# Performance work log

Hardware: AMD Instinct MI355X
Metric: run time of the kernel (lower is better)

Reference implementation:

```python
import jax, jax.numpy as jnp
import numpy as np

EPS = 1e-12  # torch F.normalize default eps


def _l2norm(t, axis=-1):
    n = jnp.sqrt(jnp.sum(t * t, axis=axis, keepdims=True))
    return t / jnp.maximum(n, EPS)


def setup_inputs() -> dict:
    key = jax.random.key(0)
    ks = jax.random.split(key, 5)
    B, N, C, H = 8, 4096, 1024, 16
    x = jax.random.normal(ks[0], (B, N, C), dtype=jnp.float32)
    # nn.Linear(dim, 3*dim, bias=False): weight [3C, C]; we store transposed [C, 3C]
    w_qkv = jax.random.normal(ks[1], (C, 3 * C), dtype=jnp.float32) * (1.0 / np.sqrt(C))
    temperature = jnp.ones((H, 1, 1), dtype=jnp.float32)
    w_proj = jax.random.normal(ks[2], (C, C), dtype=jnp.float32) * (1.0 / np.sqrt(C))
    b_proj = jax.random.normal(ks[3], (C,), dtype=jnp.float32) * 0.01
    return {"x": x, "w_qkv": w_qkv, "temperature": temperature,
            "w_proj": w_proj, "b_proj": b_proj}


def reference(x, w_qkv, temperature, w_proj, b_proj):
    B, N, C = x.shape
    H = temperature.shape[0]
    dh = C // H
    # qkv: [B, N, 3C] -> [B, N, 3, H, dh] -> q/k/v each [B, H, dh, N]
    qkv = (x @ w_qkv).reshape(B, N, 3, H, dh).transpose(2, 0, 3, 4, 1)
    q, k, v = qkv[0], qkv[1], qkv[2]
    # L2-normalize over token axis (last dim)
    q = _l2norm(q)
    k = _l2norm(k)
    # channel-channel attention: [B, H, dh, dh]
    attn = jnp.einsum("bhdn,bhen->bhde", q, k) * temperature  # temp broadcasts [H,1,1]
    attn = jax.nn.softmax(attn, axis=-1)
    # weighted sum over channels: [B, H, dh, N] -> [B, N, C]
    out = jnp.einsum("bhde,bhen->bhdn", attn, v).transpose(0, 3, 1, 2).reshape(B, N, C)
    return out @ w_proj + b_proj
```

## Files before the change

### kernel.cpp

```cpp
#include <hip/hip_runtime.h>
#include <cstdint>

typedef unsigned short u16;
typedef unsigned int u32;
typedef __attribute__((ext_vector_type(8))) short bf16x8;
typedef __attribute__((ext_vector_type(4))) float f32x4;

typedef const u32 __attribute__((address_space(1)))* gp_t;
typedef u32 __attribute__((address_space(3)))* lp_t;

__device__ __forceinline__ u16 f2bf(float f) {
    union { float f; u32 u; } v; v.f = f;
    u32 r = v.u + 0x7FFFu + ((v.u >> 16) & 1u);
    return (u16)(r >> 16);
}
__device__ __forceinline__ float bf2f(u16 h) {
    union { u32 u; float f; } v; v.u = ((u32)h) << 16;
    return v.f;
}

__global__ void k_pack_x(const float* __restrict__ x, u16* __restrict__ xb, int n4) {
    int stride = gridDim.x * blockDim.x;
    for (int i = blockIdx.x * blockDim.x + threadIdx.x; i < n4; i += stride) {
        float4 v = ((const float4*)x)[i];
        ushort4 o;
        o.x = f2bf(v.x); o.y = f2bf(v.y); o.z = f2bf(v.z); o.w = f2bf(v.w);
        ((ushort4*)xb)[i] = o;
    }
}

__global__ void k_transpose_w(const float* __restrict__ src, u16* __restrict__ dst, int ncols) {
    __shared__ float t[64][65];
    int ntn = ncols >> 6;
    int kb = (blockIdx.x / ntn) * 64;
    int nb = (blockIdx.x % ntn) * 64;
    for (int i = threadIdx.x; i < 4096; i += 256) {
        int r = i >> 6, c = i & 63;
        t[r][c] = src[(long)(kb + r) * ncols + nb + c];
    }
    __syncthreads();
    for (int i = threadIdx.x; i < 4096; i += 256) {
        int r = i >> 6, c = i & 63;
        dst[(long)(nb + r) * 1024 + kb + c] = f2bf(t[c][r]);
    }
}

__global__ __launch_bounds__(256) void k_pack_wv(const float* __restrict__ wqkv, u16* __restrict__ wvb) {
    const int idx = blockIdx.x * 256 + threadIdx.x;
    const int cin = idx >> 7, e0 = (idx & 127) * 8;
    const float4 v1 = *(const float4*)(wqkv + (long)cin * 3072 + 2048 + e0);
    const float4 v2 = *(const float4*)(wqkv + (long)cin * 3072 + 2048 + e0 + 4);
    u16 u[8];
    u[0] = f2bf(v1.x); u[1] = f2bf(v1.y); u[2] = f2bf(v1.z); u[3] = f2bf(v1.w);
    u[4] = f2bf(v2.x); u[5] = f2bf(v2.y); u[6] = f2bf(v2.z); u[7] = f2bf(v2.w);
    *(uint4*)(wvb + (long)cin * 1024 + e0) = *(const uint4*)u;
}

template<int EPI>
__global__ __launch_bounds__(512, 2) void k_gemm(
    const u16* __restrict__ A, const u16* __restrict__ Bt,
    int nTilesN,
    u16* __restrict__ qkT, u16* __restrict__ v_tm,
    float* __restrict__ outp, const float* __restrict__ bias)
{
    __shared__ uint4 smem4[8704];
    u16* sm = (u16*)smem4;

    const int tid = threadIdx.x;
    const int wid = tid >> 6, lane = tid & 63;
    const int wr = wid >> 2, wc = wid & 3;
    const int fr = lane & 15, sl = lane >> 4;

    const int nwg = gridDim.x;
    const int cpx = nwg >> 3;
    const int logical = (blockIdx.x & 7) * cpx + (blockIdx.x >> 3);

    const int bn = logical % nTilesN;
    const long m0 = (long)(logical / nTilesN) * 256;
    const int n0 = bn * 256;

    const int srow = wid * 32 + (lane >> 2);
    const int kswz = (((lane & 3) ^ ((srow >> 1) & 3)) << 3);
    const u16* gA = A + (m0 + srow) * 1024L + kswz;
    const u16* gB = Bt + ((long)n0 + srow) * 1024L + kswz;
    const int ldst = wid * 1024;

    const int fxor = ((sl ^ ((fr >> 1) & 3)) << 3);
    const int aBase = (wr * 128 + fr) * 32 + fxor;
    const int bBase = 32768 + (wc * 64 + fr) * 32 + fxor;

    f32x4 acc[8][4];
#pragma unroll
    for (int i = 0; i < 8; ++i)
#pragma unroll
        for (int j = 0; j < 4; ++j) acc[i][j] = (f32x4){0.f, 0.f, 0.f, 0.f};

#define STAGE_A(d, kh, ts) do { \
    const u16* g_ = gA + (ts) * 64 + (kh) * 32; \
    u16* l_ = sm + (d) * 16384 + (kh) * 8192 + ldst; \
    __builtin_amdgcn_global_load_lds((gp_t)g_, (lp_t)l_, 16, 0, 0); \
    __builtin_amdgcn_global_load_lds((gp_t)(g_ + 16 * 1024), (lp_t)(l_ + 512), 16, 0, 0); \
} while (0)
#define STAGE_B(d, kh, ts) do { \
    const u16* g_ = gB + (ts) * 64 + (kh) * 32; \
    u16* l_ = sm + 32768 + (d) * 16384 + (kh) * 8192 + ldst; \
    __builtin_amdgcn_global_load_lds((gp_t)g_, (lp_t)l_, 16, 0, 0); \
    __builtin_amdgcn_global_load_lds((gp_t)(g_ + 16 * 1024), (lp_t)(l_ + 512), 16, 0, 0); \
} while (0)

    STAGE_A(0, 0, 0); STAGE_B(0, 0, 0);
    STAGE_A(0, 1, 0); STAGE_B(0, 1, 0);
    STAGE_A(1, 0, 1); STAGE_B(1, 0, 1);
    asm volatile("s_waitcnt vmcnt(8)" ::: "memory");
    __builtin_amdgcn_s_barrier();

    bf16x8 afX[4], afY[4], bfX[4], bfY[4];
#pragma unroll
    for (int ni = 0; ni < 4; ++ni) bfX[ni] = *(const bf16x8*)(sm + bBase + ni * 512);
#pragma unroll
    for (int mi = 0; mi < 4; ++mi) afX[mi] = *(const bf16x8*)(sm + aBase + mi * 512);

#pragma unroll 2
    for (int T = 0; T < 16; ++T) {
        const int d = T & 1;
        const int t1 = (T + 1 < 16) ? T + 1 : 15;
        const int t2 = (T + 2 < 16) ? T + 2 : 15;
        const int base = d * 16384;
        const int nbase = (d ^ 1) * 16384;

#pragma unroll
        for (int mi = 0; mi < 4; ++mi)
            afY[mi] = *(const bf16x8*)(sm + aBase + (4 + mi) * 512 + base);
        STAGE_A(d ^ 1, 1, t1);
        asm volatile("s_waitcnt vmcnt(6)" ::: "memory");
        __builtin_amdgcn_s_barrier();
        __builtin_amdgcn_s_setprio(1);
#pragma unroll
// ... 9 lines not shown
            bfY[ni] = *(const bf16x8*)(sm + bBase + ni * 512 + base + 8192);
#pragma unroll
        for (int mi = 0; mi < 4; ++mi)
            afX[mi] = *(const bf16x8*)(sm + aBase + mi * 512 + base + 8192);
        STAGE_B(d ^ 1, 1, t1);
        __builtin_amdgcn_s_barrier();
        __builtin_amdgcn_s_setprio(1);
#pragma unroll
        for (int mi = 0; mi < 4; ++mi)
#pragma unroll
            for (int ni = 0; ni < 4; ++ni)
                acc[mi + 4][ni] = __builtin_amdgcn_mfma_f32_16x16x32_bf16(afY[mi], bfX[ni], acc[mi + 4][ni], 0, 0, 0);
        __builtin_amdgcn_s_setprio(0);
        __builtin_amdgcn_s_barrier();

#pragma unroll
        for (int mi = 0; mi < 4; ++mi)
            afY[mi] = *(const bf16x8*)(sm + aBase + (4 + mi) * 512 + base + 8192);
        STAGE_A(d, 0, t2);
        asm volatile("s_waitcnt vmcnt(6)" ::: "memory");
        __builtin_amdgcn_s_barrier();
        __builtin_amdgcn_s_setprio(1);
#pragma unroll
        for (int mi = 0; mi < 4; ++mi)
#pragma unroll
            for (int ni = 0; ni < 4; ++ni)
                acc[mi][ni] = __builtin_amdgcn_mfma_f32_16x16x32_bf16(afX[mi], bfY[ni], acc[mi][ni], 0, 0, 0);
        __builtin_amdgcn_s_setprio(0);
        __builtin_amdgcn_s_barrier();

#pragma unroll
        for (int ni = 0; ni < 4; ++ni)
            bfX[ni] = *(const bf16x8*)(sm + bBase + ni * 512 + nbase);
#pragma unroll
        for (int mi = 0; mi < 4; ++mi)
            afX[mi] = *(const bf16x8*)(sm + aBase + mi * 512 + nbase);
        STAGE_B(d, 0, t2);
        __builtin_amdgcn_s_barrier();
        __builtin_amdgcn_s_setprio(1);
#pragma unroll
        for (int mi = 0; mi < 4; ++mi)
#pragma unroll
            for (int ni = 0; ni < 4; ++ni)
                acc[mi + 4][ni] = __builtin_amdgcn_mfma_f32_16x16x32_bf16(afY[mi], bfY[ni], acc[mi + 4][ni], 0, 0, 0);
        __builtin_amdgcn_s_setprio(0);
        __builtin_amdgcn_s_barrier();
    }
#undef STAGE_A
#undef STAGE_B
    asm volatile("s_waitcnt vmcnt(0)" ::: "memory");
    __syncthreads();

    if (EPI == 0) {
        const long b = m0 >> 12;
        const int tok0 = (int)(m0 & 4095);
        u16* piece = sm + wid * 8704;
#pragma unroll
        for (int mi = 0; mi < 8; ++mi)
#pragma unroll
            for (int ni = 0; ni < 4; ++ni) {
                const int ch = ni * 16 + fr;
                const int tk = mi * 16 + sl * 4;
                ushort4 w;
                w.x = f2bf(acc[mi][ni][0]); w.y = f2bf(acc[mi][ni][1]);
                w.z = f2bf(acc[mi][ni][2]); w.w = f2bf(acc[mi][ni][3]);
                *(ushort4*)(piece + ch * 136 + tk) = w;
            }
        __syncthreads();
#pragma unroll
        for (int i = 0; i < 16; ++i) {
            const int chunk = i * 512 + tid;
            const int row = chunk >> 4, c16 = chunk & 15;
            const int p = row >> 6, chl = row & 63;
            const int wrp = p >> 2, wcp = p & 3;
            const uint4 v = *(const uint4*)(sm + p * 8704 + chl * 136 + c16 * 8);
            *(uint4*)(qkT + ((b * 2048 + n0 + wcp * 64 + chl) * 4096L + tok0 + wrp * 128 + c16 * 8)) = v;
        }
    }
}

__global__ __launch_bounds__(512, 2) void k_gram(
    const u16* __restrict__ qkT, float* __restrict__ gram_part, float* __restrict__ sq_part)
{
    __shared__ u16 lQ[64 * 256];
    __shared__ u16 lK[64 * 256];

    const int blk = blockIdx.x;
    const int seg = blk & 15;
    const int bh = blk >> 4;
    const int b = bh >> 4, h = bh & 15;
    const int tid = threadIdx.x;
    const int wid = tid >> 6, lane = tid & 63;

    {
        const int r2 = lane >> 5;
        const int slot = lane & 31;
        const int rbase = wid * 8;
#pragma unroll
        for (int i = 0; i < 4; ++i) {
            const int r = rbase + i * 2 + r2;
            const int col = seg * 256 + ((slot ^ (r & 7)) << 3);
            const u16* gq = qkT + ((long)(b * 2048 + h * 64 + r)) * 4096 + col;
            const u16* gk = qkT + ((long)(b * 2048 + 1024 + h * 64 + r)) * 4096 + col;
            __builtin_amdgcn_global_load_lds((gp_t)gq, (lp_t)(lQ + (rbase + i * 2) * 256), 16, 0, 0);
            __builtin_amdgcn_global_load_lds((gp_t)gk, (lp_t)(lK + (rbase + i * 2) * 256), 16, 0, 0);
        }
    }
    __syncthreads();

    {
        const int row = tid >> 2, q4 = tid & 3;
        const u16* src = (row < 64 ? lQ + row * 256 : lK + (row - 64) * 256) + q4 * 64;
        float s = 0.f;
#pragma unroll
        for (int i = 0; i < 8; ++i) {
            uint4 v = *(const uint4*)(src + i * 8);
            float a0, a1;
            a0 = bf2f((u16)(v.x & 0xFFFF)); a1 = bf2f((u16)(v.x >> 16)); s += a0 * a0 + a1 * a1;
            a0 = bf2f((u16)(v.y & 0xFFFF)); a1 = bf2f((u16)(v.y >> 16)); s += a0 * a0 + a1 * a1;
            a0 = bf2f((u16)(v.z & 0xFFFF)); a1 = bf2f((u16)(v.z >> 16)); s += a0 * a0 + a1 * a1;
            a0 = bf2f((u16)(v.w & 0xFFFF)); a1 = bf2f((u16)(v.w >> 16)); s += a0 * a0 + a1 * a1;
        }
        s += __shfl_xor(s, 1);
        s += __shfl_xor(s, 2);
        if (q4 == 0) sq_part[(long)blk * 128 + row] = s;
    }

    const int mrow = wid >> 1, npair = wid & 1;
    const int fr = lane & 15, sl = lane >> 4;
    f32x4 acc[2];
    acc[0] = (f32x4){0.f, 0.f, 0.f, 0.f};
    acc[1] = (f32x4){0.f, 0.f, 0.f, 0.f};
#pragma unroll
    for (int ks = 0; ks < 8; ++ks) {
        const int ra = mrow * 16 + fr;
        const bf16x8 a = *(const bf16x8*)(lQ + ra * 256 + (((ks * 4 + sl) ^ (ra & 7)) << 3));
#pragma unroll
        for (int ni = 0; ni < 2; ++ni) {
            const int rb = npair * 32 + ni * 16 + fr;
            const bf16x8 bb = *(const bf16x8*)(lK + rb * 256 + (((ks * 4 + sl) ^ (rb & 7)) << 3));
            acc[ni] = __builtin_amdgcn_mfma_f32_16x16x32_bf16(a, bb, acc[ni], 0, 0, 0);
        }
    }
    float* gp = gram_part + (long)blk * 4096;
#pragma unroll
    for (int ni = 0; ni < 2; ++ni)
#pragma unroll
        for (int r = 0; r < 4; ++r)
            gp[(mrow * 16 + sl * 4 + r) * 64 + npair * 32 + ni * 16 + fr] = acc[ni][r];
}

__global__ __launch_bounds__(256) void k_smax(
    const float* __restrict__ gram_part, const float* __restrict__ sq_part,
    const float* __restrict__ temperature, u16* __restrict__ attn_g)
{
    const int row = blockIdx.x * 4 + (threadIdx.x >> 6);
    const int e = threadIdx.x & 63;
    const int bh = row >> 6, d = row & 63;
    const int h = bh & 15;
    float raw = 0.f, sqq = 0.f, sqk = 0.f;
    const float* gp = gram_part + (long)bh * 16 * 4096 + d * 64 + e;
    const float* sp = sq_part + (long)bh * 16 * 128;
#pragma unroll
    for (int s = 0; s < 16; ++s) {
        raw += gp[s * 4096];
        sqq += sp[s * 128 + d];
        sqk += sp[s * 128 + 64 + e];
    }
    const float rq = 1.f / fmaxf(sqrtf(sqq), 1e-12f);
    const float rk = 1.f / fmaxf(sqrtf(sqk), 1e-12f);
    const float v = raw * rq * rk * temperature[h];
    float mx = v;
#pragma unroll
    for (int o = 32; o; o >>= 1) mx = fmaxf(mx, __shfl_xor(mx, o));
    const float p = __expf(v - mx);
    float sum = p;
#pragma unroll
    for (int o = 32; o; o >>= 1) sum += __shfl_xor(sum, o);
    attn_g[(long)row * 64 + e] = f2bf(p / sum);
}

__global__ __launch_bounds__(256) void k_wmix(
    const u16* __restrict__ attn_g, const u16* __restrict__ wpT, u16* __restrict__ wmix)
{
    __shared__ u16 lA[64 * 72];
    __shared__ u16 lB[256 * 64];

    const int blk = blockIdx.x;
    const int nseg = blk & 3, bh = blk >> 2;
    const int b = bh >> 4, h = bh & 15;
    const int tid = threadIdx.x;
    const int wid = tid >> 6, lane = tid & 63;
    const int fr = lane & 15, sl = lane >> 4;

#pragma unroll
    for (int i = 0; i < 8; ++i) {
        const int cc = wid * 8 + i;
        const int row = cc * 8 + (lane >> 3);
        const int slot = lane & 7;
        const u16* g = wpT + (long)(nseg * 256 + row) * 1024 + h * 64 + ((slot ^ (row & 7)) << 3);
        __builtin_amdgcn_global_load_lds((gp_t)g, (lp_t)(lB + cc * 512), 16, 0, 0);
    }
    {
        const u16* src = attn_g + (long)bh * 4096;
        for (int i = tid; i < 4096; i += 256) {
            const int d = i >> 6, e = i & 63;
            lA[e * 72 + d] = src[i];
        }
    }
    __syncthreads();

    f32x4 acc[4][4];
#pragma unroll
    for (int i = 0; i < 4; ++i)
#pragma unroll
        for (int j = 0; j < 4; ++j) acc[i][j] = (f32x4){0.f, 0.f, 0.f, 0.f};

#pragma unroll
    for (int ks = 0; ks < 2; ++ks) {
        bf16x8 a[4], bb[4];
#pragma unroll
        for (int mi = 0; mi < 4; ++mi)
            a[mi] = *(const bf16x8*)(lA + (mi * 16 + fr) * 72 + ks * 32 + sl * 8);
#pragma unroll
        for (int ni = 0; ni < 4; ++ni) {
            const int rb = wid * 64 + ni * 16 + fr;
            bb[ni] = *(const bf16x8*)(lB + rb * 64 + (((ks * 4 + sl) ^ (rb & 7)) << 3));
        }
#pragma unroll
        for (int mi = 0; mi < 4; ++mi)
#pragma unroll
            for (int ni = 0; ni < 4; ++ni)
                acc[mi][ni] = __builtin_amdgcn_mfma_f32_16x16x32_bf16(a[mi], bb[ni], acc[mi][ni], 0, 0, 0);
    }

    u16* dst = wmix + ((long)b << 20);
#pragma unroll
    for (int mi = 0; mi < 4; ++mi)
#pragma unroll
        for (int ni = 0; ni < 4; ++ni) {
            const int cout = nseg * 256 + wid * 64 + ni * 16 + fr;
            const int e0 = mi * 16 + sl * 4;
            ushort4 w;
            w.x = f2bf(acc[mi][ni][0]); w.y = f2bf(acc[mi][ni][1]);
            w.z = f2bf(acc[mi][ni][2]); w.w = f2bf(acc[mi][ni][3]);
            *(ushort4*)(dst + (long)cout * 1024 + h * 64 + e0) = w;
        }
}

__global__ __launch_bounds__(256) void k_g128(
    const u16* __restrict__ A, long Ab, const u16* __restrict__ Bt, long Bs,
    u16* __restrict__ C, long Cb, int K, int MT, int NT)
{
    __shared__ u16 sm[8192];
    __shared__ u16 lC[128 * 136];

    const int tid = threadIdx.x;
    const int wid = tid >> 6, lane = tid & 63;
    const int wr = wid >> 1, wc = wid & 1;
    const int fr = lane & 15, sl = lane >> 4;

    const int nwg = gridDim.x;
    const int logical = (blockIdx.x & 7) * (nwg >> 3) + (blockIdx.x >> 3);

    const int b = logical / (MT * NT);
    const int r = logical % (MT * NT);
    const int i0 = r / NT, j0 = r % NT;
    const int m0 = i0 * 128, n0 = j0 * 128;
    const u16* Abp = A + (long)b * Ab;
    const u16* Bbp = Bt + (long)b * Bs;
    u16* Cbp = C + (long)b * Cb;

    const int srow = lane >> 2;
    const int sslot = lane & 3;

    f32x4 acc[4][4];
#pragma unroll
    for (int i = 0; i < 4; ++i)
#pragma unroll
        for (int j = 0; j < 4; ++j) acc[i][j] = (f32x4){0.f, 0.f, 0.f, 0.f};

    for (int kt = 0; kt < K; kt += 32) {
        __syncthreads();
#pragma unroll
        for (int i = 0; i < 2; ++i) {
            const int row = wid * 32 + i * 16 + srow;
            const int swz = (sslot ^ ((row >> 1) & 3)) << 3;
            const u16* ga = Abp + (long)(m0 + row) * K + kt + swz;
            const u16* gb = Bbp + (long)(n0 + row) * K + kt + swz;
            __builtin_amdgcn_global_load_lds((gp_t)ga, (lp_t)(sm + (wid * 2 + i) * 512), 16, 0, 0);
            __builtin_amdgcn_global_load_lds((gp_t)gb, (lp_t)(sm + 4096 + (wid * 2 + i) * 512), 16, 0, 0);
        }
        __syncthreads();
        bf16x8 af[4], bfr[4];
#pragma unroll
        for (int mi = 0; mi < 4; ++mi) {
            const int row = wr * 64 + mi * 16 + fr;
            af[mi] = *(const bf16x8*)(sm + row * 32 + ((sl ^ ((row >> 1) & 3)) << 3));
        }
#pragma unroll
        for (int ni = 0; ni < 4; ++ni) {
            const int row = wc * 64 + ni * 16 + fr;
            bfr[ni] = *(const bf16x8*)(sm + 4096 + row * 32 + ((sl ^ ((row >> 1) & 3)) << 3));
        }
#pragma unroll
        for (int mi = 0; mi < 4; ++mi)
#pragma unroll
            for (int ni = 0; ni < 4; ++ni)
                acc[mi][ni] = __builtin_amdgcn_mfma_f32_16x16x32_bf16(af[mi], bfr[ni], acc[mi][ni], 0, 0, 0);
    }
    __syncthreads();

#pragma unroll
    for (int mi = 0; mi < 4; ++mi)
#pragma unroll
        for (int ni = 0; ni < 4; ++ni) {
            const int ch = wc * 64 + ni * 16 + fr;
            const int tk = wr * 64 + mi * 16 + sl * 4;
#pragma unroll
            for (int rr = 0; rr < 4; ++rr)
                lC[(tk + rr) * 136 + ch] = f2bf(acc[mi][ni][rr]);
        }
    __syncthreads();
    {
        const int tk = tid >> 1, half = tid & 1;
        const u16* sp = lC + tk * 136 + half * 64;
        u16* dp = Cbp + (long)(m0 + tk) * 1024 + n0 + half * 64;
#pragma unroll
        for (int i = 0; i < 8; ++i) ((uint4*)dp)[i] = ((const uint4*)sp)[i];
    }
}

__global__ __launch_bounds__(512, 2) void k_gemm256f(
    const u16* __restrict__ A, long Ab, const u16* __restrict__ Bt, long Bs,
    int MT, int NT, float* __restrict__ cF, long Cb, const float* __restrict__ bias)
{
    __shared__ uint4 smem4[8704];
    u16* sm = (u16*)smem4;

    const int tid = threadIdx.x;
    const int wid = tid >> 6, lane = tid & 63;
    const int wr = wid >> 2, wc = wid & 3;
    const int fr = lane & 15, sl = lane >> 4;

    const int nwg = gridDim.x;
    const int logical = (blockIdx.x & 7) * (nwg >> 3) + (blockIdx.x >> 3);
    const int b = logical / (MT * NT);
    const int rem = logical % (MT * NT);
    const int mt = rem / NT, nt = rem % NT;
    const long m0 = (long)mt * 256;
    const int n0 = nt * 256;

    const int srow = wid * 32 + (lane >> 2);
    const int kswz = (((lane & 3) ^ ((srow >> 1) & 3)) << 3);
    const u16* gA = A + (long)b * Ab + (m0 + srow) * 1024L + kswz;
    const u16* gB = Bt + (long)b * Bs + ((long)n0 + srow) * 1024L + kswz;
    const int ldst = wid * 1024;

    const int fxor = ((sl ^ ((fr >> 1) & 3)) << 3);
    const int aBase = (wr * 128 + fr) * 32 + fxor;
    const int bBase = 32768 + (wc * 64 + fr) * 32 + fxor;

    f32x4 acc[8][4];
#pragma unroll
    for (int i = 0; i < 8; ++i)
#pragma unroll
        for (int j = 0; j < 4; ++j) acc[i][j] = (f32x4){0.f, 0.f, 0.f, 0.f};

#define STAGE_A(d, kh, ts) do { \
    const u16* g_ = gA + (ts) * 64 + (kh) * 32; \
    u16* l_ = sm + (d) * 16384 + (kh) * 8192 + ldst; \
    __builtin_amdgcn_global_load_lds((gp_t)g_, (lp_t)l_, 16, 0, 0); \
    __builtin_amdgcn_global_load_lds((gp_t)(g_ + 16 * 1024), (lp_t)(l_ + 512), 16, 0, 0); \
} while (0)
#define STAGE_B(d, kh, ts) do { \
    const u16* g_ = gB + (ts) * 64 + (kh) * 32; \
    u16* l_ = sm + 32768 + (d) * 16384 + (kh) * 8192 + ldst; \
    __builtin_amdgcn_global_load_lds((gp_t)g_, (lp_t)l_, 16, 0, 0); \
    __builtin_amdgcn_global_load_lds((gp_t)(g_ + 16 * 1024), (lp_t)(l_ + 512), 16, 0, 0); \
} while (0)

    STAGE_A(0, 0, 0); STAGE_B(0, 0, 0);
    STAGE_A(0, 1, 0); STAGE_B(0, 1, 0);
    STAGE_A(1, 0, 1); STAGE_B(1, 0, 1);
    asm volatile("s_waitcnt vmcnt(8)" ::: "memory");
    __builtin_amdgcn_s_barrier();

    bf16x8 afX[4], afY[4], bfX[4], bfY[4];
#pragma unroll
    for (int ni = 0; ni < 4; ++ni) bfX[ni] = *(const bf16x8*)(sm + bBase + ni * 512);
#pragma unroll
    for (int mi = 0; mi < 4; ++mi) afX[mi] = *(const bf16x8*)(sm + aBase + mi * 512);

#pragma unroll 2
    for (int T = 0; T < 16; ++T) {
        const int d = T & 1;
        const int t1 = (T + 1 < 16) ? T + 1 : 15;
        const int t2 = (T + 2 < 16) ? T + 2 : 15;
        const int base = d * 16384;
        const int nbase = (d ^ 1) * 16384;

#pragma unroll
        for (int mi = 0; mi < 4; ++mi)
            afY[mi] = *(const bf16x8*)(sm + aBase + (4 + mi) * 512 + base);
        STAGE_A(d ^ 1, 1, t1);
        asm volatile("s_waitcnt vmcnt(6)" ::: "memory");
        __builtin_amdgcn_s_barrier();
        __builtin_amdgcn_s_setprio(1);
#pragma unroll
        for (int mi = 0; mi < 4; ++mi)
#pragma unroll
            for (int ni = 0; ni < 4; ++ni)
                acc[mi][ni] = __builtin_amdgcn_mfma_f32_16x16x32_bf16(afX[mi], bfX[ni], acc[mi][ni], 0, 0, 0);
        __builtin_amdgcn_s_setprio(0);
        __builtin_amdgcn_s_barrier();

#pragma unroll
        for (int ni = 0; ni < 4; ++ni)
            bfY[ni] = *(const bf16x8*)(sm + bBase + ni * 512 + base + 8192);
#pragma unroll
        for (int mi = 0; mi < 4; ++mi)
            afX[mi] = *(const bf16x8*)(sm + aBase + mi * 512 + base + 8192);
        STAGE_B(d ^ 1, 1, t1);
        __builtin_amdgcn_s_barrier();
        __builtin_amdgcn_s_setprio(1);
#pragma unroll
        for (int mi = 0; mi < 4; ++mi)
#pragma unroll
            for (int ni = 0; ni < 4; ++ni)
                acc[mi + 4][ni] = __builtin_amdgcn_mfma_f32_16x16x32_bf16(afY[mi], bfX[ni], acc[mi + 4][ni], 0, 0, 0);
        __builtin_amdgcn_s_setprio(0);
        __builtin_amdgcn_s_barrier();

#pragma unroll
        for (int mi = 0; mi < 4; ++mi)
            afY[mi] = *(const bf16x8*)(sm + aBase + (4 + mi) * 512 + base + 8192);
        STAGE_A(d, 0, t2);
        asm volatile("s_waitcnt vmcnt(6)" ::: "memory");
        __builtin_amdgcn_s_barrier();
        __builtin_amdgcn_s_setprio(1);
#pragma unroll
        for (int mi = 0; mi < 4; ++mi)
#pragma unroll
            for (int ni = 0; ni < 4; ++ni)
                acc[mi][ni] = __builtin_amdgcn_mfma_f32_16x16x32_bf16(afX[mi], bfY[ni], acc[mi][ni], 0, 0, 0);
        __builtin_amdgcn_s_setprio(0);
        __builtin_amdgcn_s_barrier();

#pragma unroll
        for (int ni = 0; ni < 4; ++ni)
            bfX[ni] = *(const bf16x8*)(sm + bBase + ni * 512 + nbase);
#pragma unroll
        for (int mi = 0; mi < 4; ++mi)
            afX[mi] = *(const bf16x8*)(sm + aBase + mi * 512 + nbase);
        STAGE_B(d, 0, t2);
        __builtin_amdgcn_s_barrier();
        __builtin_amdgcn_s_setprio(1);
#pragma unroll
        for (int mi = 0; mi < 4; ++mi)
#pragma unroll
            for (int ni = 0; ni < 4; ++ni)
                acc[mi + 4][ni] = __builtin_amdgcn_mfma_f32_16x16x32_bf16(afY[mi], bfY[ni], acc[mi + 4][ni], 0, 0, 0);
        __builtin_amdgcn_s_setprio(0);
        __builtin_amdgcn_s_barrier();
    }
#undef STAGE_A
#undef STAGE_B
    asm volatile("s_waitcnt vmcnt(0)" ::: "memory");
    __syncthreads();

    float* cbase = cF + (long)b * Cb;
    float bi[4];
#pragma unroll
    for (int ni = 0; ni < 4; ++ni) bi[ni] = bias[n0 + wc * 64 + ni * 16 + fr];
#pragma unroll
    for (int pass = 0; pass < 2; ++pass) {
        float* pieceF = (float*)smem4 + wid * 4352;
        if (pass) __syncthreads();
#pragma unroll
        for (int mi2 = 0; mi2 < 4; ++mi2) {
            const int mi = pass * 4 + mi2;
#pragma unroll
            for (int ni = 0; ni < 4; ++ni) {
                const int ch = ni * 16 + fr;
                const int tk = mi2 * 16 + sl * 4;
#pragma unroll
                for (int rr = 0; rr < 4; ++rr)
                    pieceF[(tk + rr) * 68 + ch] = acc[mi][ni][rr] + bi[ni];
            }
        }
        __syncthreads();
#pragma unroll
        for (int i = 0; i < 16; ++i) {
            const int chunk = i * 512 + tid;
            const int row = chunk >> 4, c4 = chunk & 15;
            const int p = row >> 6, tk = row & 63;
            const int wrp = p >> 2, wcp = p & 3;
            const float4 v = *(const float4*)((float*)smem4 + p * 4352 + tk * 68 + c4 * 4);
            *(float4*)(cbase + (m0 + wrp * 128 + pass * 64 + tk) * 1024L + n0 + wcp * 64 + c4 * 4) = v;
        }
    }
}

extern "C" void kernel_launch(void* const* d_in, const int* in_sizes, int n_in,
                              void* d_out, int out_size, void* d_ws, size_t ws_size,
                              hipStream_t stream) {
    const float* x = (const float*)d_in[0];
    const float* w_qkv = (const float*)d_in[1];
    const float* temperature = (const float*)d_in[2];
    const float* w_proj = (const float*)d_in[3];
    const float* b_proj = (const float*)d_in[4];
    float* out = (float*)d_out;
    char* ws = (char*)d_ws;

    u16* wqT    = (u16*)(ws);
    u16* wpT    = (u16*)(ws + 6291456);
    u16* wvb    = (u16*)(ws + 8388608);
    u16* xt     = (u16*)(ws + 10485760);
    u16* qkT    = (u16*)(ws + 77594624);
    float* gram_part = (float*)(ws + 211812352);
    float* sq_part   = (float*)(ws + 245366784);
    u16* attn_g = (u16*)(ws + 246415360);
    u16* wmix   = (u16*)(ws + 247463936);
    u16* wfinT  = (u16*)(ws + 211812352);

    k_pack_x<<<2048, 256, 0, stream>>>(x, xt, 8388608);
    k_transpose_w<<<768, 256, 0, stream>>>(w_qkv, wqT, 3072);
    k_transpose_w<<<256, 256, 0, stream>>>(w_proj, wpT, 1024);
    k_pack_wv<<<512, 256, 0, stream>>>(w_qkv, wvb);
    k_gemm<0><<<1024, 512, 0, stream>>>(xt, wqT, 8, qkT, nullptr, nullptr, nullptr);
    k_gram<<<2048, 512, 0, stream>>>(qkT, gram_part, sq_part);
    k_smax<<<2048, 256, 0, stream>>>(gram_part, sq_part, temperature, attn_g);
    k_wmix<<<512, 256, 0, stream>>>(attn_g, wpT, wmix);
    k_g128<<<512, 256, 0, stream>>>(wmix, 1048576L, wvb, 0L, wfinT, 1048576L, 1024, 8, 8);
    k_gemm256f<<<512, 512, 0, stream>>>(xt, 4194304L, wfinT, 1048576L, 16, 4, out, 4194304L, b_proj);
}
```

Baseline: 358.6 us.

## Compute gram via input covariance X^T X instead of materializing Q/K projections

Replaces the large QK projection GEMM over all tokens with a symmetric per-batch covariance S = X^T X (1024x1024), then forms U = S·Wqk and gets the Q·K gram and the row norms as Wq^T·U contractions. A new pack kernel writes x in both token-major and channel-major bf16 layouts so the symmetric GEMM can read it. The goal is to drop the B·N×2C projection, its writeback and the partial-gram reductions. In exchange it adds a transpose pass over x and an extra intermediate, and accumulating S and U in bf16 may change numerical accuracy.

```diff
diff --git a/kernel.cpp b/kernel.cpp
--- a/kernel.cpp
+++ b/kernel.cpp
@@ -19,13 +19,40 @@
     return v.f;
 }
 
-__global__ void k_pack_x(const float* __restrict__ x, u16* __restrict__ xb, int n4) {
-    int stride = gridDim.x * blockDim.x;
-    for (int i = blockIdx.x * blockDim.x + threadIdx.x; i < n4; i += stride) {
-        float4 v = ((const float4*)x)[i];
-        ushort4 o;
-        o.x = f2bf(v.x); o.y = f2bf(v.y); o.z = f2bf(v.z); o.w = f2bf(v.w);
-        ((ushort4*)xb)[i] = o;
+__global__ __launch_bounds__(256) void k_pack2(const float* __restrict__ x,
+                                               u16* __restrict__ xt, u16* __restrict__ xc) {
+    __shared__ u16 tb[64][72];
+    const int blk = blockIdx.x;
+    const int tt = blk >> 4, ct = blk & 15;
+    const long tok0 = (long)tt * 64;
+    const int ch0 = ct * 64;
+    const int tid = threadIdx.x;
+    const int row = tid >> 2, cq = tid & 3;
+#pragma unroll
+    for (int jj = 0; jj < 4; ++jj) {
+        const float4 v = *(const float4*)(x + (tok0 + row) * 1024 + ch0 + cq * 16 + jj * 4);
+        tb[row][cq * 16 + jj * 4 + 0] = f2bf(v.x);
+        tb[row][cq * 16 + jj * 4 + 1] = f2bf(v.y);
+        tb[row][cq * 16 + jj * 4 + 2] = f2bf(v.z);
+        tb[row][cq * 16 + jj * 4 + 3] = f2bf(v.w);
+    }
+    __syncthreads();
+#pragma unroll
+    for (int s = 0; s < 2; ++s) {
+        const int c = s * 256 + tid;
+        const int r2 = c >> 3, col8 = c & 7;
+        *(uint4*)(xt + (tok0 + r2) * 1024 + ch0 + col8 * 8) = *(const uint4*)(&tb[r2][col8 * 8]);
+    }
+    const int b = (int)(tok0 >> 12);
+    const int nin = (int)(tok0 & 4095);
+#pragma unroll
+    for (int s = 0; s < 2; ++s) {
+        const int c = s * 256 + tid;
+        const int crow = c >> 3, t8 = c & 7;
+        u16 u[8];
+#pragma unroll
+        for (int k = 0; k < 8; ++k) u[k] = tb[t8 * 8 + k][crow];
+        *(uint4*)(xc + ((long)b * 1024 + ch0 + crow) * 4096 + nin + t8 * 8) = *(const uint4*)u;
     }
 }
 
@@ -56,12 +83,125 @@
     *(uint4*)(wvb + (long)cin * 1024 + e0) = *(const uint4*)u;
 }
 
+template<int SYM>
+__global__ __launch_bounds__(256) void k_g128(
+    const u16* __restrict__ A, long Ab, const u16* __restrict__ Bt, long Bs,
+    u16* __restrict__ C, long Cb, int K, int MT, int NT)
+{
+    __shared__ u16 sm[8192];
+    __shared__ u16 lC[128 * 136];
+
+    const int tid = threadIdx.x;
+    const int wid = tid >> 6, lane = tid & 63;
+    const int wr = wid >> 1, wc = wid & 1;
+    const int fr = lane & 15, sl = lane >> 4;
+
+    const int nwg = gridDim.x;
+    const int logical = (blockIdx.x & 7) * (nwg >> 3) + (blockIdx.x >> 3);
+
+    int b, i0, j0;
+    if (SYM) {
+        const int per = MT * (MT + 1) / 2;
+        b = logical / per;
+        int t = logical % per;
+        int i = 0;
+        while (t >= MT - i) { t -= MT - i; ++i; }
+        i0 = i; j0 = i + t;
+    } else {
+        b = logical / (MT * NT);
+        const int r = logical % (MT * NT);
+        i0 = r / NT; j0 = r % NT;
+    }
+    const int m0 = i0 * 128, n0 = j0 * 128;
+    const u16* Abp = A + (long)b * Ab;
+    const u16* Bbp = Bt + (long)b * Bs;
+    u16* Cbp = C + (long)b * Cb;
+
+    const int srow = lane >> 2;
+    const int sslot = lane & 3;
+
+    f32x4 acc[4][4];
+#pragma unroll
+    for (int i = 0; i < 4; ++i)
+#pragma unroll
+        for (int j = 0; j < 4; ++j) acc[i][j] = (f32x4){0.f, 0.f, 0.f, 0.f};
+
+    for (int kt = 0; kt < K; kt += 32) {
+        __syncthreads();
+#pragma unroll
+        for (int i = 0; i < 2; ++i) {
+            const int row = wid * 32 + i * 16 + srow;
+            const int swz = (sslot ^ ((row >> 1) & 3)) << 3;
+            const u16* ga = Abp + (long)(m0 + row) * K + kt + swz;
+            const u16* gb = Bbp + (long)(n0 + row) * K + kt + swz;
+            __builtin_amdgcn_global_load_lds((gp_t)ga, (lp_t)(sm + (wid * 2 + i) * 512), 16, 0, 0);
+            __builtin_amdgcn_global_load_lds((gp_t)gb, (lp_t)(sm + 4096 + (wid * 2 + i) * 512), 16, 0, 0);
+        }
+        __syncthreads();
+        bf16x8 af[4], bfr[4];
+#pragma unroll
+        for (int mi = 0; mi < 4; ++mi) {
+            const int row = wr * 64 + mi * 16 + fr;
+            af[mi] = *(const bf16x8*)(sm + row * 32 + ((sl ^ ((row >> 1) & 3)) << 3));
+        }
+#pragma unroll
+        for (int ni = 0; ni < 4; ++ni) {
+            const int row = wc * 64 + ni * 16 + fr;
+            bfr[ni] = *(const bf16x8*)(sm + 4096 + row * 32 + ((sl ^ ((row >> 1) & 3)) << 3));
+        }
+#pragma unroll
+        for (int mi = 0; mi < 4; ++mi)
+#pragma unroll
+            for (int ni = 0; ni < 4; ++ni)
+                acc[mi][ni] = __builtin_amdgcn_mfma_f32_16x16x32_bf16(af[mi], bfr[ni], acc[mi][ni], 0, 0, 0);
+    }
+    __syncthreads();
+
+#pragma unroll
+    for (int mi = 0; mi < 4; ++mi)
+#pragma unroll
+        for (int ni = 0; ni < 4; ++ni) {
+            const int ch = wc * 64 + ni * 16 + fr;
+            const int tk = wr * 64 + mi * 16 + sl * 4;
+#pragma unroll
+            for (int rr = 0; rr < 4; ++rr)
+                lC[(tk + rr) * 136 + ch] = f2bf(acc[mi][ni][rr]);
+        }
+    __syncthreads();
+    {
+        const int tk = tid >> 1, half = tid & 1;
+        const u16* sp = lC + tk * 136 + half * 64;
+        u16* dp = Cbp + (long)(m0 + tk) * 1024 + n0 + half * 64;
+#pragma unroll
+        for (int i = 0; i < 8; ++i) ((uint4*)dp)[i] = ((const uint4*)sp)[i];
+    }
+    if (SYM && i0 != j0) {
+        __syncthreads();
+#pragma unroll
+        for (int mi = 0; mi < 4; ++mi)
+#pragma unroll
+            for (int ni = 0; ni < 4; ++ni) {
+                const int ch = wc * 64 + ni * 16 + fr;
+                const int tk = wr * 64 + mi * 16 + sl * 4;
+                ushort4 w;
+                w.x = f2bf(acc[mi][ni][0]); w.y = f2bf(acc[mi][ni][1]);
+                w.z = f2bf(acc[mi][ni][2]); w.w = f2bf(acc[mi][ni][3]);
+                *(ushort4*)(lC + ch * 136 + tk) = w;
+            }
+        __syncthreads();
+        const int rw = tid >> 1, half = tid & 1;
+        const u16* sp = lC + rw * 136 + half * 64;
+        u16* dp = Cbp + (long)(n0 + rw) * 1024 + m0 + half * 64;
+#pragma unroll
+        for (int i = 0; i < 8; ++i) ((uint4*)dp)[i] = ((const uint4*)sp)[i];
+    }
+}
+
 template<int EPI>
-__global__ __launch_bounds__(512, 2) void k_gemm(
-    const u16* __restrict__ A, const u16* __restrict__ Bt,
-    int nTilesN,
-    u16* __restrict__ qkT, u16* __restrict__ v_tm,
-    float* __restrict__ outp, const float* __restrict__ bias)
+__global__ __launch_bounds__(512, 2) void k_gemm256(
+    const u16* __restrict__ A, long Ab, const u16* __restrict__ Bt, long Bs,
+    int MT, int NT,
+    u16* __restrict__ cB, float* __restrict__ cF, long Cb, const float* __restrict__ bias)
 {
     __shared__ uint4 smem4[8704];
     u16* sm = (u16*)smem4;
@@ -72,17 +212,17 @@
     const int fr = lane & 15, sl = lane >> 4;
 
     const int nwg = gridDim.x;
-    const int cpx = nwg >> 3;
-    const int logical = (blockIdx.x & 7) * cpx + (blockIdx.x >> 3);
-
-    const int bn = logical % nTilesN;
-    const long m0 = (long)(logical / nTilesN) * 256;
-    const int n0 = bn * 256;
+    const int logical = (blockIdx.x & 7) * (nwg >> 3) + (blockIdx.x >> 3);
+    const int b = logical / (MT * NT);
+    const int rem = logical % (MT * NT);
+    const int mt = rem / NT, nt = rem % NT;
+    const long m0 = (long)mt * 256;
+    const int n0 = nt * 256;
 
     const int srow = wid * 32 + (lane >> 2);
     const int kswz = (((lane & 3) ^ ((srow >> 1) & 3)) << 3);
-    const u16* gA = A + (m0 + srow) * 1024L + kswz;
-    const u16* gB = Bt + ((long)n0 + srow) * 1024L + kswz;
+    const u16* gA = A + (long)b * Ab + (m0 + srow) * 1024L + kswz;
+    const u16* gB = Bt + (long)b * Bs + ((long)n0 + srow) * 1024L + kswz;
     const int ldst = wid * 1024;
 
     const int fxor = ((sl ^ ((fr >> 1) & 3)) << 3);
@@ -198,8 +338,7 @@
     __syncthreads();
 
     if (EPI == 0) {
-        const long b = m0 >> 12;
-        const int tok0 = (int)(m0 & 4095);
+        u16* cbase = cB + (long)b * Cb;
         u16* piece = sm + wid * 8704;
 #pragma unroll
         for (int mi = 0; mi < 8; ++mi)
@@ -207,123 +346,130 @@
             for (int ni = 0; ni < 4; ++ni) {
                 const int ch = ni * 16 + fr;
                 const int tk = mi * 16 + sl * 4;
-                ushort4 w;
-                w.x = f2bf(acc[mi][ni][0]); w.y = f2bf(acc[mi][ni][1]);
-                w.z = f2bf(acc[mi][ni][2]); w.w = f2bf(acc[mi][ni][3]);
-                *(ushort4*)(piece + ch * 136 + tk) = w;
+#pragma unroll
+                for (int rr = 0; rr < 4; ++rr)
+                    piece[(tk + rr) * 68 + ch] = f2bf(acc[mi][ni][rr]);
             }
         __syncthreads();
 #pragma unroll
-        for (int i = 0; i < 16; ++i) {
+        for (int i = 0; i < 32; ++i) {
             const int chunk = i * 512 + tid;
-            const int row = chunk >> 4, c16 = chunk & 15;
-            const int p = row >> 6, chl = row & 63;
+            const int row = chunk >> 4, c8 = chunk & 15;
+            const int p = row >> 7, tk = row & 127;
             const int wrp = p >> 2, wcp = p & 3;
-            const uint4 v = *(const uint4*)(sm + p * 8704 + chl * 136 + c16 * 8);
-            *(uint4*)(qkT + ((b * 2048 + n0 + wcp * 64 + chl) * 4096L + tok0 + wrp * 128 + c16 * 8)) = v;
-        }
-    }
-}
-
-__global__ __launch_bounds__(512, 2) void k_gram(
-    const u16* __restrict__ qkT, float* __restrict__ gram_part, float* __restrict__ sq_part)
+            const uint2 v = *(const uint2*)(sm + p * 8704 + tk * 68 + c8 * 4);
+            *(uint2*)(cbase + (m0 + wrp * 128 + tk) * 1024L + n0 + wcp * 64 + c8 * 4) = v;
+        }
+    } else {
+        float* cbase = cF + (long)b * Cb;
+        float bi[4];
+#pragma unroll
+        for (int ni = 0; ni < 4; ++ni) bi[ni] = bias[n0 + wc * 64 + ni * 16 + fr];
+#pragma unroll
+        for (int pass = 0; pass < 2; ++pass) {
+            float* pieceF = (float*)smem4 + wid * 4352;
+            if (pass) __syncthreads();
+#pragma unroll
+            for (int mi2 = 0; mi2 < 4; ++mi2) {
+                const int mi = pass * 4 + mi2;
+#pragma unroll
+                for (int ni = 0; ni < 4; ++ni) {
+                    const int ch = ni * 16 + fr;
+                    const int tk = mi2 * 16 + sl * 4;
+#pragma unroll
+                    for (int rr = 0; rr < 4; ++rr)
+                        pieceF[(tk + rr) * 68 + ch] = acc[mi][ni][rr] + bi[ni];
+                }
+            }
+            __syncthreads();
+#pragma unroll
+            for (int i = 0; i < 16; ++i) {
+                const int chunk = i * 512 + tid;
+                const int row = chunk >> 4, c4 = chunk & 15;
+                const int p = row >> 6, tk = row & 63;
+                const int wrp = p >> 2, wcp = p & 3;
+                const float4 v = *(const float4*)((float*)smem4 + p * 4352 + tk * 68 + c4 * 4);
+                *(float4*)(cbase + (m0 + wrp * 128 + pass * 64 + tk) * 1024L + n0 + wcp * 64 + c4 * 4) = v;
+            }
+        }
+    }
+}
+
+__global__ __launch_bounds__(256) void k_gram2(
+    const u16* __restrict__ wqT, const u16* __restrict__ Ut,
+    const float* __restrict__ temperature, u16* __restrict__ attn_g)
 {
-    __shared__ u16 lQ[64 * 256];
-    __shared__ u16 lK[64 * 256];
-
-    const int blk = blockIdx.x;
-    const int seg = blk & 15;
-    const int bh = blk >> 4;
+    __shared__ float lS[64 * 65];
+    __shared__ float lsq[128];
+
+    const int bh = blockIdx.x;
     const int b = bh >> 4, h = bh & 15;
     const int tid = threadIdx.x;
     const int wid = tid >> 6, lane = tid & 63;
+    const int fr = lane & 15, sl = lane >> 4;
 
     {
-        const int r2 = lane >> 5;
-        const int slot = lane & 31;
-        const int rbase = wid * 8;
-#pragma unroll
-        for (int i = 0; i < 4; ++i) {
-            const int r = rbase + i * 2 + r2;
-            const int col = seg * 256 + ((slot ^ (r & 7)) << 3);
-            const u16* gq = qkT + ((long)(b * 2048 + h * 64 + r)) * 4096 + col;
-            const u16* gk = qkT + ((long)(b * 2048 + 1024 + h * 64 + r)) * 4096 + col;
-            __builtin_amdgcn_global_load_lds((gp_t)gq, (lp_t)(lQ + (rbase + i * 2) * 256), 16, 0, 0);
-            __builtin_amdgcn_global_load_lds((gp_t)gk, (lp_t)(lK + (rbase + i * 2) * 256), 16, 0, 0);
-        }
-    }
-    __syncthreads();
-
-    {
-        const int row = tid >> 2, q4 = tid & 3;
-        const u16* src = (row < 64 ? lQ + row * 256 : lK + (row - 64) * 256) + q4 * 64;
+        const int row = tid >> 1, half = tid & 1;
+        const int j = (row < 64) ? (h * 64 + row) : (1024 + h * 64 + (row - 64));
+        const u16* pa = wqT + (long)j * 1024 + half * 512;
+        const u16* pb = Ut + ((long)b * 2048 + j) * 1024 + half * 512;
         float s = 0.f;
-#pragma unroll
-        for (int i = 0; i < 8; ++i) {
-            uint4 v = *(const uint4*)(src + i * 8);
-            float a0, a1;
-            a0 = bf2f((u16)(v.x & 0xFFFF)); a1 = bf2f((u16)(v.x >> 16)); s += a0 * a0 + a1 * a1;
-            a0 = bf2f((u16)(v.y & 0xFFFF)); a1 = bf2f((u16)(v.y >> 16)); s += a0 * a0 + a1 * a1;
-            a0 = bf2f((u16)(v.z & 0xFFFF)); a1 = bf2f((u16)(v.z >> 16)); s += a0 * a0 + a1 * a1;
-            a0 = bf2f((u16)(v.w & 0xFFFF)); a1 = bf2f((u16)(v.w >> 16)); s += a0 * a0 + a1 * a1;
+#pragma unroll 4
+        for (int i = 0; i < 64; ++i) {
+            const uint4 a = *(const uint4*)(pa + i * 8);
+            const uint4 bv = *(const uint4*)(pb + i * 8);
+            s += bf2f((u16)(a.x & 0xFFFF)) * bf2f((u16)(bv.x & 0xFFFF));
+            s += bf2f((u16)(a.x >> 16))    * bf2f((u16)(bv.x >> 16));
+            s += bf2f((u16)(a.y & 0xFFFF)) * bf2f((u16)(bv.y & 0xFFFF));
+            s += bf2f((u16)(a.y >> 16))    * bf2f((u16)(bv.y >> 16));
+            s += bf2f((u16)(a.z & 0xFFFF)) * bf2f((u16)(bv.z & 0xFFFF));
+            s += bf2f((u16)(a.z >> 16))    * bf2f((u16)(bv.z >> 16));
+            s += bf2f((u16)(a.w & 0xFFFF)) * bf2f((u16)(bv.w & 0xFFFF));
+            s += bf2f((u16)(a.w >> 16))    * bf2f((u16)(bv.w >> 16));
         }
         s += __shfl_xor(s, 1);
-        s += __shfl_xor(s, 2);
-        if (q4 == 0) sq_part[(long)blk * 128 + row] = s;
-    }
-
-    const int mrow = wid >> 1, npair = wid & 1;
-    const int fr = lane & 15, sl = lane >> 4;
-    f32x4 acc[2];
-    acc[0] = (f32x4){0.f, 0.f, 0.f, 0.f};
-    acc[1] = (f32x4){0.f, 0.f, 0.f, 0.f};
-#pragma unroll
-    for (int ks = 0; ks < 8; ++ks) {
-        const int ra = mrow * 16 + fr;
-        const bf16x8 a = *(const bf16x8*)(lQ + ra * 256 + (((ks * 4 + sl) ^ (ra & 7)) << 3));
-#pragma unroll
-        for (int ni = 0; ni < 2; ++ni) {
-            const int rb = npair * 32 + ni * 16 + fr;
-            const bf16x8 bb = *(const bf16x8*)(lK + rb * 256 + (((ks * 4 + sl) ^ (rb & 7)) << 3));
+        if (half == 0) lsq[row] = s;
+    }
+
+    const int d0 = wid * 16;
+    f32x4 acc[4];
+#pragma unroll
+    for (int i = 0; i < 4; ++i) acc[i] = (f32x4){0.f, 0.f, 0.f, 0.f};
+
+    const u16* aRow = wqT + (long)(h * 64 + d0 + fr) * 1024 + sl * 8;
+    const u16* bRow = Ut + ((long)b * 2048 + 1024 + h * 64 + fr) * 1024 + sl * 8;
+#pragma unroll 4
+    for (int kb = 0; kb < 32; ++kb) {
+        const bf16x8 a = *(const bf16x8*)(aRow + kb * 32);
+#pragma unroll
+        for (int ni = 0; ni < 4; ++ni) {
+            const bf16x8 bb = *(const bf16x8*)(bRow + (long)ni * 16384 + kb * 32);
             acc[ni] = __builtin_amdgcn_mfma_f32_16x16x32_bf16(a, bb, acc[ni], 0, 0, 0);
         }
     }
-    float* gp = gram_part + (long)blk * 4096;
-#pragma unroll
-    for (int ni = 0; ni < 2; ++ni)
-#pragma unroll
-        for (int r = 0; r < 4; ++r)
-            gp[(mrow * 16 + sl * 4 + r) * 64 + npair * 32 + ni * 16 + fr] = acc[ni][r];
-}
-
-__global__ __launch_bounds__(256) void k_smax(
-    const float* __restrict__ gram_part, const float* __restrict__ sq_part,
-    const float* __restrict__ temperature, u16* __restrict__ attn_g)
-{
-    const int row = blockIdx.x * 4 + (threadIdx.x >> 6);
-    const int e = threadIdx.x & 63;
-    const int bh = row >> 6, d = row & 63;
-    const int h = bh & 15;
-    float raw = 0.f, sqq = 0.f, sqk = 0.f;
-    const float* gp = gram_part + (long)bh * 16 * 4096 + d * 64 + e;
-    const float* sp = sq_part + (long)bh * 16 * 128;
-#pragma unroll
-    for (int s = 0; s < 16; ++s) {
-        raw += gp[s * 4096];
-        sqq += sp[s * 128 + d];
-        sqk += sp[s * 128 + 64 + e];
-    }
-    const float rq = 1.f / fmaxf(sqrtf(sqq), 1e-12f);
-    const float rk = 1.f / fmaxf(sqrtf(sqk), 1e-12f);
-    const float v = raw * rq * rk * temperature[h];
-    float mx = v;
-#pragma unroll
-    for (int o = 32; o; o >>= 1) mx = fmaxf(mx, __shfl_xor(mx, o));
-    const float p = __expf(v - mx);
-    float sum = p;
-#pragma unroll
-    for (int o = 32; o; o >>= 1) sum += __shfl_xor(sum, o);
-    attn_g[(long)row * 64 + e] = f2bf(p / sum);
+#pragma unroll
+    for (int ni = 0; ni < 4; ++ni)
+#pragma unroll
+        for (int rr = 0; rr < 4; ++rr)
+            lS[(d0 + sl * 4 + rr) * 65 + ni * 16 + fr] = acc[ni][rr];
+    __syncthreads();
+
+    const float temp = temperature[h];
+    const float rk = 1.f / fmaxf(sqrtf(lsq[64 + lane]), 1e-12f);
+#pragma unroll 2
+    for (int i = 0; i < 16; ++i) {
+        const int d = wid * 16 + i;
+        const float rq = 1.f / fmaxf(sqrtf(lsq[d]), 1e-12f);
+        const float v = lS[d * 65 + lane] * rq * rk * temp;
+        float mx = v;
+#pragma unroll
+        for (int o = 32; o; o >>= 1) mx = fmaxf(mx, __shfl_xor(mx, o));
+        const float p = __expf(v - mx);
+        float sum = p;
+#pragma unroll
+        for (int o = 32; o; o >>= 1) sum += __shfl_xor(sum, o);
+        attn_g[(long)bh * 4096 + d * 64 + lane] = f2bf(p / sum);
+    }
 }
 
 __global__ __launch_bounds__(256) void k_wmix(
@@ -392,260 +538,6 @@
             w.z = f2bf(acc[mi][ni][2]); w.w = f2bf(acc[mi][ni][3]);
             *(ushort4*)(dst + (long)cout * 1024 + h * 64 + e0) = w;
         }
-}
-
-__global__ __launch_bounds__(256) void k_g128(
-    const u16* __restrict__ A, long Ab, const u16* __restrict__ Bt, long Bs,
-    u16* __restrict__ C, long Cb, int K, int MT, int NT)
-{
-    __shared__ u16 sm[8192];
-    __shared__ u16 lC[128 * 136];
-
-    const int tid = threadIdx.x;
-    const int wid = tid >> 6, lane = tid & 63;
-    const int wr = wid >> 1, wc = wid & 1;
-    const int fr = lane & 15, sl = lane >> 4;
-
-    const int nwg = gridDim.x;
-    const int logical = (blockIdx.x & 7) * (nwg >> 3) + (blockIdx.x >> 3);
-
-    const int b = logical / (MT * NT);
-    const int r = logical % (MT * NT);
-    const int i0 = r / NT, j0 = r % NT;
-    const int m0 = i0 * 128, n0 = j0 * 128;
-    const u16* Abp = A + (long)b * Ab;
-    const u16* Bbp = Bt + (long)b * Bs;
-    u16* Cbp = C + (long)b * Cb;
-
-    const int srow = lane >> 2;
-    const int sslot = lane & 3;
-
-    f32x4 acc[4][4];
-#pragma unroll
-    for (int i = 0; i < 4; ++i)
-#pragma unroll
-        for (int j = 0; j < 4; ++j) acc[i][j] = (f32x4){0.f, 0.f, 0.f, 0.f};
-
-    for (int kt = 0; kt < K; kt += 32) {
-        __syncthreads();
-#pragma unroll
-        for (int i = 0; i < 2; ++i) {
-            const int row = wid * 32 + i * 16 + srow;
-            const int swz = (sslot ^ ((row >> 1) & 3)) << 3;
-            const u16* ga = Abp + (long)(m0 + row) * K + kt + swz;
-            const u16* gb = Bbp + (long)(n0 + row) * K + kt + swz;
-            __builtin_amdgcn_global_load_lds((gp_t)ga, (lp_t)(sm + (wid * 2 + i) * 512), 16, 0, 0);
-            __builtin_amdgcn_global_load_lds((gp_t)gb, (lp_t)(sm + 4096 + (wid * 2 + i) * 512), 16, 0, 0);
-        }
-        __syncthreads();
-        bf16x8 af[4], bfr[4];
-#pragma unroll
-        for (int mi = 0; mi < 4; ++mi) {
-            const int row = wr * 64 + mi * 16 + fr;
-            af[mi] = *(const bf16x8*)(sm + row * 32 + ((sl ^ ((row >> 1) & 3)) << 3));
-        }
-#pragma unroll
-        for (int ni = 0; ni < 4; ++ni) {
-            const int row = wc * 64 + ni * 16 + fr;
-            bfr[ni] = *(const bf16x8*)(sm + 4096 + row * 32 + ((sl ^ ((row >> 1) & 3)) << 3));
-        }
-#pragma unroll
-        for (int mi = 0; mi < 4; ++mi)
-#pragma unroll
-            for (int ni = 0; ni < 4; ++ni)
-                acc[mi][ni] = __builtin_amdgcn_mfma_f32_16x16x32_bf16(af[mi], bfr[ni], acc[mi][ni], 0, 0, 0);
-    }
-    __syncthreads();
-
-#pragma unroll
-    for (int mi = 0; mi < 4; ++mi)
-#pragma unroll
-        for (int ni = 0; ni < 4; ++ni) {
-            const int ch = wc * 64 + ni * 16 + fr;
-            const int tk = wr * 64 + mi * 16 + sl * 4;
-#pragma unroll
-            for (int rr = 0; rr < 4; ++rr)
-                lC[(tk + rr) * 136 + ch] = f2bf(acc[mi][ni][rr]);
-        }
-    __syncthreads();
-    {
-        const int tk = tid >> 1, half = tid & 1;
-        const u16* sp = lC + tk * 136 + half * 64;
-        u16* dp = Cbp + (long)(m0 + tk) * 1024 + n0 + half * 64;
-#pragma unroll
-        for (int i = 0; i < 8; ++i) ((uint4*)dp)[i] = ((const uint4*)sp)[i];
-    }
-}
-
-__global__ __launch_bounds__(512, 2) void k_gemm256f(
-    const u16* __restrict__ A, long Ab, const u16* __restrict__ Bt, long Bs,
-    int MT, int NT, float* __restrict__ cF, long Cb, const float* __restrict__ bias)
-{
-    __shared__ uint4 smem4[8704];
-    u16* sm = (u16*)smem4;
-
-    const int tid = threadIdx.x;
-    const int wid = tid >> 6, lane = tid & 63;
-    const int wr = wid >> 2, wc = wid & 3;
-    const int fr = lane & 15, sl = lane >> 4;
-
-    const int nwg = gridDim.x;
-    const int logical = (blockIdx.x & 7) * (nwg >> 3) + (blockIdx.x >> 3);
-    const int b = logical / (MT * NT);
-    const int rem = logical % (MT * NT);
-    const int mt = rem / NT, nt = rem % NT;
-    const long m0 = (long)mt * 256;
-    const int n0 = nt * 256;
-
-    const int srow = wid * 32 + (lane >> 2);
-    const int kswz = (((lane & 3) ^ ((srow >> 1) & 3)) << 3);
-    const u16* gA = A + (long)b * Ab + (m0 + srow) * 1024L + kswz;
-    const u16* gB = Bt + (long)b * Bs + ((long)n0 + srow) * 1024L + kswz;
-    const int ldst = wid * 1024;
-
-    const int fxor = ((sl ^ ((fr >> 1) & 3)) << 3);
-    const int aBase = (wr * 128 + fr) * 32 + fxor;
-    const int bBase = 32768 + (wc * 64 + fr) * 32 + fxor;
-
-    f32x4 acc[8][4];
-#pragma unroll
-    for (int i = 0; i < 8; ++i)
-#pragma unroll
-        for (int j = 0; j < 4; ++j) acc[i][j] = (f32x4){0.f, 0.f, 0.f, 0.f};
-
-#define STAGE_A(d, kh, ts) do { \
-    const u16* g_ = gA + (ts) * 64 + (kh) * 32; \
-    u16* l_ = sm + (d) * 16384 + (kh) * 8192 + ldst; \
-    __builtin_amdgcn_global_load_lds((gp_t)g_, (lp_t)l_, 16, 0, 0); \
-    __builtin_amdgcn_global_load_lds((gp_t)(g_ + 16 * 1024), (lp_t)(l_ + 512), 16, 0, 0); \
-} while (0)
-#define STAGE_B(d, kh, ts) do { \
-    const u16* g_ = gB + (ts) * 64 + (kh) * 32; \
-    u16* l_ = sm + 32768 + (d) * 16384 + (kh) * 8192 + ldst; \
-    __builtin_amdgcn_global_load_lds((gp_t)g_, (lp_t)l_, 16, 0, 0); \
-    __builtin_amdgcn_global_load_lds((gp_t)(g_ + 16 * 1024), (lp_t)(l_ + 512), 16, 0, 0); \
-} while (0)
-
-    STAGE_A(0, 0, 0); STAGE_B(0, 0, 0);
-    STAGE_A(0, 1, 0); STAGE_B(0, 1, 0);
-    STAGE_A(1, 0, 1); STAGE_B(1, 0, 1);
-    asm volatile("s_waitcnt vmcnt(8)" ::: "memory");
-    __builtin_amdgcn_s_barrier();
-
-    bf16x8 afX[4], afY[4], bfX[4], bfY[4];
-#pragma unroll
-    for (int ni = 0; ni < 4; ++ni) bfX[ni] = *(const bf16x8*)(sm + bBase + ni * 512);
-#pragma unroll
-    for (int mi = 0; mi < 4; ++mi) afX[mi] = *(const bf16x8*)(sm + aBase + mi * 512);
-
-#pragma unroll 2
-    for (int T = 0; T < 16; ++T) {
-        const int d = T & 1;
-        const int t1 = (T + 1 < 16) ? T + 1 : 15;
-        const int t2 = (T + 2 < 16) ? T + 2 : 15;
-        const int base = d * 16384;
-        const int nbase = (d ^ 1) * 16384;
-
-#pragma unroll
-        for (int mi = 0; mi < 4; ++mi)
-            afY[mi] = *(const bf16x8*)(sm + aBase + (4 + mi) * 512 + base);
-        STAGE_A(d ^ 1, 1, t1);
-        asm volatile("s_waitcnt vmcnt(6)" ::: "memory");
-        __builtin_amdgcn_s_barrier();
-        __builtin_amdgcn_s_setprio(1);
-#pragma unroll
-        for (int mi = 0; mi < 4; ++mi)
-#pragma unroll
-            for (int ni = 0; ni < 4; ++ni)
-                acc[mi][ni] = __builtin_amdgcn_mfma_f32_16x16x32_bf16(afX[mi], bfX[ni], acc[mi][ni], 0, 0, 0);
-        __builtin_amdgcn_s_setprio(0);
-        __builtin_amdgcn_s_barrier();
-
-#pragma unroll
-        for (int ni = 0; ni < 4; ++ni)
-            bfY[ni] = *(const bf16x8*)(sm + bBase + ni * 512 + base + 8192);
-#pragma unroll
-        for (int mi = 0; mi < 4; ++mi)
-            afX[mi] = *(const bf16x8*)(sm + aBase + mi * 512 + base + 8192);
-        STAGE_B(d ^ 1, 1, t1);
-        __builtin_amdgcn_s_barrier();
-        __builtin_amdgcn_s_setprio(1);
-#pragma unroll
-        for (int mi = 0; mi < 4; ++mi)
-#pragma unroll
-            for (int ni = 0; ni < 4; ++ni)
-                acc[mi + 4][ni] = __builtin_amdgcn_mfma_f32_16x16x32_bf16(afY[mi], bfX[ni], acc[mi + 4][ni], 0, 0, 0);
-        __builtin_amdgcn_s_setprio(0);
-        __builtin_amdgcn_s_barrier();
-
-#pragma unroll
-        for (int mi = 0; mi < 4; ++mi)
-            afY[mi] = *(const bf16x8*)(sm + aBase + (4 + mi) * 512 + base + 8192);
-        STAGE_A(d, 0, t2);
-        asm volatile("s_waitcnt vmcnt(6)" ::: "memory");
-        __builtin_amdgcn_s_barrier();
-        __builtin_amdgcn_s_setprio(1);
-#pragma unroll
-        for (int mi = 0; mi < 4; ++mi)
-#pragma unroll
-            for (int ni = 0; ni < 4; ++ni)
-                acc[mi][ni] = __builtin_amdgcn_mfma_f32_16x16x32_bf16(afX[mi], bfY[ni], acc[mi][ni], 0, 0, 0);
-        __builtin_amdgcn_s_setprio(0);
-        __builtin_amdgcn_s_barrier();
-
-#pragma unroll
-        for (int ni = 0; ni < 4; ++ni)
-            bfX[ni] = *(const bf16x8*)(sm + bBase + ni * 512 + nbase);
-#pragma unroll
-        for (int mi = 0; mi < 4; ++mi)
-            afX[mi] = *(const bf16x8*)(sm + aBase + mi * 512 + nbase);
-        STAGE_B(d, 0, t2);
-        __builtin_amdgcn_s_barrier();
-        __builtin_amdgcn_s_setprio(1);
-#pragma unroll
-        for (int mi = 0; mi < 4; ++mi)
-#pragma unroll
-            for (int ni = 0; ni < 4; ++ni)
-                acc[mi + 4][ni] = __builtin_amdgcn_mfma_f32_16x16x32_bf16(afY[mi], bfY[ni], acc[mi + 4][ni], 0, 0, 0);
-        __builtin_amdgcn_s_setprio(0);
-        __builtin_amdgcn_s_barrier();
-    }
-#undef STAGE_A
-#undef STAGE_B
-    asm volatile("s_waitcnt vmcnt(0)" ::: "memory");
-    __syncthreads();
-
-    float* cbase = cF + (long)b * Cb;
-    float bi[4];
-#pragma unroll
-    for (int ni = 0; ni < 4; ++ni) bi[ni] = bias[n0 + wc * 64 + ni * 16 + fr];
-#pragma unroll
-    for (int pass = 0; pass < 2; ++pass) {
-        float* pieceF = (float*)smem4 + wid * 4352;
-        if (pass) __syncthreads();
-#pragma unroll
-        for (int mi2 = 0; mi2 < 4; ++mi2) {
-            const int mi = pass * 4 + mi2;
-#pragma unroll
-            for (int ni = 0; ni < 4; ++ni) {
-                const int ch = ni * 16 + fr;
-                const int tk = mi2 * 16 + sl * 4;
-#pragma unroll
-                for (int rr = 0; rr < 4; ++rr)
-                    pieceF[(tk + rr) * 68 + ch] = acc[mi][ni][rr] + bi[ni];
-            }
-        }
-        __syncthreads();
-#pragma unroll
-        for (int i = 0; i < 16; ++i) {
-            const int chunk = i * 512 + tid;
-            const int row = chunk >> 4, c4 = chunk & 15;
-            const int p = row >> 6, tk = row & 63;
-            const int wrp = p >> 2, wcp = p & 3;
-            const float4 v = *(const float4*)((float*)smem4 + p * 4352 + tk * 68 + c4 * 4);
-            *(float4*)(cbase + (m0 + wrp * 128 + pass * 64 + tk) * 1024L + n0 + wcp * 64 + c4 * 4) = v;
-        }
-    }
 }
 
 extern "C" void kernel_launch(void* const* d_in, const int* in_sizes, int n_in,
@@ -663,21 +555,21 @@
     u16* wpT    = (u16*)(ws + 6291456);
     u16* wvb    = (u16*)(ws + 8388608);
     u16* xt     = (u16*)(ws + 10485760);
-    u16* qkT    = (u16*)(ws + 77594624);
-    float* gram_part = (float*)(ws + 211812352);
-    float* sq_part   = (float*)(ws + 245366784);
-    u16* attn_g = (u16*)(ws + 246415360);
-    u16* wmix   = (u16*)(ws + 247463936);
-    u16* wfinT  = (u16*)(ws + 211812352);
-
-    k_pack_x<<<2048, 256, 0, stream>>>(x, xt, 8388608);
+    u16* xc     = (u16*)(ws + 77594624);
+    u16* S      = (u16*)(ws + 144703488);
+    u16* Ut     = (u16*)(ws + 161480704);
+    u16* attn_g = (u16*)(ws + 195035136);
+    u16* wmix   = (u16*)(ws + 196083712);
+    u16* wfinT  = (u16*)(ws + 212860928);
+
+    k_pack2<<<8192, 256, 0, stream>>>(x, xt, xc);
     k_transpose_w<<<768, 256, 0, stream>>>(w_qkv, wqT, 3072);
     k_transpose_w<<<256, 256, 0, stream>>>(w_proj, wpT, 1024);
     k_pack_wv<<<512, 256, 0, stream>>>(w_qkv, wvb);
-    k_gemm<0><<<1024, 512, 0, stream>>>(xt, wqT, 8, qkT, nullptr, nullptr, nullptr);
-    k_gram<<<2048, 512, 0, stream>>>(qkT, gram_part, sq_part);
-    k_smax<<<2048, 256, 0, stream>>>(gram_part, sq_part, temperature, attn_g);
+    k_g128<1><<<288, 256, 0, stream>>>(xc, 4194304L, xc, 4194304L, S, 1048576L, 4096, 8, 0);
+    k_gemm256<0><<<256, 512, 0, stream>>>(wqT, 0L, S, 1048576L, 8, 4, Ut, nullptr, 2097152L, nullptr);
+    k_gram2<<<128, 256, 0, stream>>>(wqT, Ut, temperature, attn_g);
     k_wmix<<<512, 256, 0, stream>>>(attn_g, wpT, wmix);
-    k_g128<<<512, 256, 0, stream>>>(wmix, 1048576L, wvb, 0L, wfinT, 1048576L, 1024, 8, 8);
-    k_gemm256f<<<512, 512, 0, stream>>>(xt, 4194304L, wfinT, 1048576L, 16, 4, out, 4194304L, b_proj);
-}
+    k_g128<0><<<512, 256, 0, stream>>>(wmix, 1048576L, wvb, 0L, wfinT, 1048576L, 1024, 8, 8);
+    k_gemm256<1><<<512, 512, 0, stream>>>(xt, 4194304L, wfinT, 1048576L, 16, 4, nullptr, out, 4194304L, b_proj);
+}
```

Result: slower. 384.7 us (+7.3%).
